# Kernel optimization log

Hardware: AMD Instinct MI355X
Metric: run time of the kernel (lower is better)

The kernel has to match this reference:

```python
import jax, jax.numpy as jnp
import numpy as np

TOPK = 8
NUM_EXPERT_GROUP = 8
TOPK_GROUP = 4
ROUTED_SCALING_FACTOR = 2.5

NUM_TOKENS = 131072
NUM_EXPERTS = 256


def setup_inputs() -> dict:
    key = jax.random.key(0)
    k1, k2 = jax.random.split(key)
    router_logits = jax.random.normal(k1, (NUM_TOKENS, NUM_EXPERTS), dtype=jnp.float32)
    correction_bias = jax.random.normal(k2, (NUM_EXPERTS,), dtype=jnp.float32)
    return {"router_logits": router_logits, "correction_bias": correction_bias}


def reference(router_logits, correction_bias):
    # Biased grouped top-k router (DeepSeek-V3 style), faithful to TopK.__call__
    logits = router_logits.astype(jnp.float32)          # [T, E]
    T, E = logits.shape
    G = NUM_EXPERT_GROUP
    experts_per_group = E // G

    scores_for_choice = logits + correction_bias[None, :]            # [T, E]
    scores_grouped = scores_for_choice.reshape(T, G, experts_per_group)
    # group score = sum of top-2 biased scores in each group
    group_scores = jnp.sum(jax.lax.top_k(scores_grouped, k=2)[0], axis=-1)  # [T, G]
    group_idx = jax.lax.top_k(group_scores, k=TOPK_GROUP)[1]                 # [T, KG]
    group_mask = jnp.clip(jax.nn.one_hot(group_idx, G).sum(axis=1), 0, 1)    # [T, G]
    score_mask = jnp.broadcast_to(group_mask[:, :, None], (T, G, experts_per_group)).reshape(T, E)
    tmp_scores = jnp.where(score_mask.astype(bool), scores_for_choice, float("-inf"))
    topk_ids = jax.lax.top_k(tmp_scores, k=TOPK)[1]                          # [T, K]
    # weights are gathered from the UNbiased logits
    topk_weights = jnp.take_along_axis(logits, topk_ids, axis=1)             # [T, K]
    # renormalize + routed scaling factor
    topk_weights = topk_weights / jnp.sum(topk_weights, axis=-1, keepdims=True)
    topk_weights = topk_weights * ROUTED_SCALING_FACTOR
    return topk_weights.astype(jnp.float32), topk_ids
```

## Files before the change

### kernel.cpp

```cpp
#include <hip/hip_runtime.h>
#include <stdint.h>
#include <math.h>

static constexpr int TOPK   = 8;
static constexpr int NGROUP = 8;
static constexpr int TOPKG  = 4;
static constexpr int NEXP   = 256;
static constexpr float RSF  = 2.5f;

static constexpr int DPP_QX1 = 0xB1;
static constexpr int DPP_QX2 = 0x4E;
static constexpr int DPP_HM  = 0x141;
static constexpr int DPP_MIR = 0x140;
static constexpr int DPP_B15 = 0x142;
static constexpr int DPP_B31 = 0x143;

template <int CTRL>
__device__ __forceinline__ float dppmov(float x) {
    int xi = __float_as_int(x);
    return __int_as_float(__builtin_amdgcn_update_dpp(xi, xi, CTRL, 0xF, 0xF, false));
}

__device__ __forceinline__ uint32_t f2sort(float f) {
    uint32_t u = __float_as_uint(f);
    return u ^ ((uint32_t)((int32_t)u >> 31) | 0x80000000u);
}

__global__ __launch_bounds__(256) void router_kernel(
    const float* __restrict__ logits,
    const float* __restrict__ bias,
    float* __restrict__ out_w,
    float* __restrict__ out_id,
    int T)
{
    const int lane  = threadIdx.x & 63;
    const int token = blockIdx.x * (blockDim.x >> 6) + (threadIdx.x >> 6);
    if (token >= T) return;

    const float* row = logits + (size_t)token * NEXP;
    float4 v = ((const float4*)row)[lane];
    float4 b = ((const float4*)bias)[lane];

    const float s0 = v.x + b.x;
    const float s1 = v.y + b.y;
    const float s2 = v.z + b.z;
    const float s3 = v.w + b.w;

    float hi01 = fmaxf(s0, s1), lo01 = fminf(s0, s1);
    float hi23 = fmaxf(s2, s3), lo23 = fminf(s2, s3);
    float m1 = fmaxf(hi01, hi23);
    float m2 = fmaxf(fminf(hi01, hi23), fmaxf(lo01, lo23));
    {
        float o1 = dppmov<DPP_QX1>(m1), o2 = dppmov<DPP_QX1>(m2);
        float n1 = fmaxf(m1, o1);
        float n2 = fmaxf(fminf(m1, o1), fmaxf(m2, o2));
        m1 = n1; m2 = n2;
    }
    {
        float o1 = dppmov<DPP_QX2>(m1), o2 = dppmov<DPP_QX2>(m2);
        float n1 = fmaxf(m1, o1);
        float n2 = fmaxf(fminf(m1, o1), fmaxf(m2, o2));
        m1 = n1; m2 = n2;
    }
    {
        float o1 = dppmov<DPP_HM>(m1), o2 = dppmov<DPP_HM>(m2);
        float n1 = fmaxf(m1, o1);
        float n2 = fmaxf(fminf(m1, o1), fmaxf(m2, o2));
        m1 = n1; m2 = n2;
    }
    const float gscore = m1 + m2;

    const int g = lane >> 3;
    const uint64_t gkey = ((uint64_t)f2sort(gscore) << 32) | (uint32_t)(7 - g);
    int rank = 0;
    #pragma unroll
    for (int j = 0; j < NGROUP; ++j) {
        uint32_t hi = (uint32_t)__builtin_amdgcn_readlane((int)(uint32_t)(gkey >> 32), j << 3);
        uint32_t lo = (uint32_t)__builtin_amdgcn_readlane((int)(uint32_t)gkey,         j << 3);
        uint64_t gj = ((uint64_t)hi << 32) | lo;
        rank += (gj > gkey) ? 1 : 0;
    }
    const bool sel = (rank < TOPKG);

    const float NEG = -INFINITY;
    float c0 = sel ? s0 : NEG;
    float c1 = sel ? s1 : NEG;
    float c2 = sel ? s2 : NEG;
    float c3 = sel ? s3 : NEG;
    const int ebase = lane << 2;

    int myid = 0;
    #pragma unroll
    for (int r = 0; r < TOPK; ++r) {
        float x = fmaxf(fmaxf(c0, c1), fmaxf(c2, c3));
        x = fmaxf(x, dppmov<DPP_QX1>(x));
        x = fmaxf(x, dppmov<DPP_QX2>(x));
        x = fmaxf(x, dppmov<DPP_HM >(x));
        x = fmaxf(x, dppmov<DPP_MIR>(x));
        x = fmaxf(x, dppmov<DPP_B15>(x));
        x = fmaxf(x, dppmov<DPP_B31>(x));
        const float smax = __int_as_float(
            __builtin_amdgcn_readlane(__float_as_int(x), 63));

        int slot = (c0 == smax) ? 0 : (c1 == smax) ? 1 : (c2 == smax) ? 2 : 3;
        int lidx = ebase | slot;
        uint64_t bal = __ballot((c0 == smax) || (c1 == smax) ||
                                (c2 == smax) || (c3 == smax));
        const int wlane = __ffsll((unsigned long long)bal) - 1;
        const int idx   = __builtin_amdgcn_readlane(lidx, wlane);

        myid = (lane == r) ? idx : myid;

        c0 = (ebase == idx    ) ? NEG : c0;
        c1 = (ebase == idx - 1) ? NEG : c1;
        c2 = (ebase == idx - 2) ? NEG : c2;
        c3 = (ebase == idx - 3) ? NEG : c3;
    }

    float w = 0.f;
    if (lane < TOPK) w = row[myid];
    float t = w;
    t += dppmov<DPP_QX1>(t);
    t += dppmov<DPP_QX2>(t);
    t += dppmov<DPP_HM >(t);

    if (lane < TOPK) {
        out_w [(size_t)token * TOPK + lane] = w / t * RSF;
        out_id[(size_t)token * TOPK + lane] = (float)myid;
    }
}

extern "C" void kernel_launch(void* const* d_in, const int* in_sizes, int n_in,
                              void* d_out, int out_size, void* d_ws, size_t ws_size,
                              hipStream_t stream) {
    const float* logits = (const float*)d_in[0];
    const float* bias   = (const float*)d_in[1];
    const int T = in_sizes[0] / NEXP;
    float* out = (float*)d_out;
    float* out_w  = out;
    float* out_id = out + (size_t)T * TOPK;

    const int waves_per_block = 256 / 64;
    const int blocks = (T + waves_per_block - 1) / waves_per_block;
    router_kernel<<<blocks, 256, 0, stream>>>(logits, bias, out_w, out_id, T);
}
```

Before: 239.8 us.

## Pre-sort per-lane scores and use ballot ranking for group selection

Each lane sorts its four biased scores with a small compare-exchange network, so each top-k round only reduces the lane's head value and shifts a packed index register on the winning lane. Group ranking now uses one shuffle plus a ballot and popcount instead of eight pairs of readlanes. The unbiased weight is rebuilt as the selected biased score minus bias[id], which replaces a scattered reload of the logits row with a bias load. This trades some per-lane sorting work for shorter loop bodies. The recovered weight can differ from the reference in the last bits because of float rounding.

After: 218.5 us. 8.9% less time.

```diff
diff --git a/kernel.cpp b/kernel.cpp
--- a/kernel.cpp
+++ b/kernel.cpp
@@ -3,7 +3,6 @@
 #include <math.h>
 
 static constexpr int TOPK   = 8;
-static constexpr int NGROUP = 8;
 static constexpr int TOPKG  = 4;
 static constexpr int NEXP   = 256;
 static constexpr float RSF  = 2.5f;
@@ -21,9 +20,11 @@
     return __int_as_float(__builtin_amdgcn_update_dpp(xi, xi, CTRL, 0xF, 0xF, false));
 }
 
-__device__ __forceinline__ uint32_t f2sort(float f) {
-    uint32_t u = __float_as_uint(f);
-    return u ^ ((uint32_t)((int32_t)u >> 31) | 0x80000000u);
+__device__ __forceinline__ void cas(float& ax, float& ay, int& ix, int& iy) {
+    bool p   = ax < ay;
+    float hi = fmaxf(ax, ay), lo = fminf(ax, ay);
+    int   nx = p ? iy : ix,   ny = p ? ix : iy;
+    ax = hi; ay = lo; ix = nx; iy = ny;
 }
 
 __global__ __launch_bounds__(256) void router_kernel(
@@ -41,10 +42,10 @@
     float4 v = ((const float4*)row)[lane];
     float4 b = ((const float4*)bias)[lane];
 
-    const float s0 = v.x + b.x;
-    const float s1 = v.y + b.y;
-    const float s2 = v.z + b.z;
-    const float s3 = v.w + b.w;
+    float s0 = v.x + b.x;
+    float s1 = v.y + b.y;
+    float s2 = v.z + b.z;
+    float s3 = v.w + b.w;
 
     float hi01 = fmaxf(s0, s1), lo01 = fminf(s0, s1);
     float hi23 = fmaxf(s2, s3), lo23 = fminf(s2, s3);
@@ -71,28 +72,34 @@
     const float gscore = m1 + m2;
 
     const int g = lane >> 3;
-    const uint64_t gkey = ((uint64_t)f2sort(gscore) << 32) | (uint32_t)(7 - g);
-    int rank = 0;
-    #pragma unroll
-    for (int j = 0; j < NGROUP; ++j) {
-        uint32_t hi = (uint32_t)__builtin_amdgcn_readlane((int)(uint32_t)(gkey >> 32), j << 3);
-        uint32_t lo = (uint32_t)__builtin_amdgcn_readlane((int)(uint32_t)gkey,         j << 3);
-        uint64_t gj = ((uint64_t)hi << 32) | lo;
-        rank += (gj > gkey) ? 1 : 0;
-    }
+    const int j = lane & 7;
+    float gj = __shfl(gscore, j << 3, 64);
+    bool beats = (gj > gscore) || (gj == gscore && j < g);
+    uint64_t bal = __ballot(beats);
+    int rank = __popcll(bal & (0xFFull << (g << 3)));
     const bool sel = (rank < TOPKG);
 
     const float NEG = -INFINITY;
-    float c0 = sel ? s0 : NEG;
-    float c1 = sel ? s1 : NEG;
-    float c2 = sel ? s2 : NEG;
-    float c3 = sel ? s3 : NEG;
+    float a0 = sel ? s0 : NEG;
+    float a1 = sel ? s1 : NEG;
+    float a2 = sel ? s2 : NEG;
+    float a3 = sel ? s3 : NEG;
     const int ebase = lane << 2;
+    int i0 = ebase, i1 = ebase + 1, i2 = ebase + 2, i3 = ebase + 3;
+    cas(a0, a1, i0, i1);
+    cas(a2, a3, i2, i3);
+    cas(a0, a2, i0, i2);
+    cas(a1, a3, i1, i3);
+    cas(a1, a2, i1, i2);
+    uint32_t ipack = (uint32_t)i0 | ((uint32_t)i1 << 8) |
+                     ((uint32_t)i2 << 16) | ((uint32_t)i3 << 24);
+    int i0cur = i0;
 
-    int myid = 0;
+    int   myid = 0;
+    float myw  = 0.f;
     #pragma unroll
     for (int r = 0; r < TOPK; ++r) {
-        float x = fmaxf(fmaxf(c0, c1), fmaxf(c2, c3));
+        float x = a0;
         x = fmaxf(x, dppmov<DPP_QX1>(x));
         x = fmaxf(x, dppmov<DPP_QX2>(x));
         x = fmaxf(x, dppmov<DPP_HM >(x));
@@ -102,23 +109,27 @@
         const float smax = __int_as_float(
             __builtin_amdgcn_readlane(__float_as_int(x), 63));
 
-        int slot = (c0 == smax) ? 0 : (c1 == smax) ? 1 : (c2 == smax) ? 2 : 3;
-        int lidx = ebase | slot;
-        uint64_t bal = __ballot((c0 == smax) || (c1 == smax) ||
-                                (c2 == smax) || (c3 == smax));
-        const int wlane = __ffsll((unsigned long long)bal) - 1;
-        const int idx   = __builtin_amdgcn_readlane(lidx, wlane);
+        uint64_t wb  = __ballot(a0 == smax);
+        const int wl = __ffsll((unsigned long long)wb) - 1;
+        const int idx = __builtin_amdgcn_readlane(i0cur, wl);
 
-        myid = (lane == r) ? idx : myid;
+        const bool mine = (lane == r);
+        myid = mine ? idx  : myid;
+        myw  = mine ? smax : myw;
 
-        c0 = (ebase == idx    ) ? NEG : c0;
-        c1 = (ebase == idx - 1) ? NEG : c1;
-        c2 = (ebase == idx - 2) ? NEG : c2;
-        c3 = (ebase == idx - 3) ? NEG : c3;
+        const bool win = (lane == wl);
+        a0 = win ? a1  : a0;
+        a1 = win ? a2  : a1;
+        a2 = win ? a3  : a2;
+        a3 = win ? NEG : a3;
+        ipack = win ? (ipack >> 8) : ipack;
+        i0cur = (int)(ipack & 255u);
     }
 
-    float w = 0.f;
-    if (lane < TOPK) w = row[myid];
+    float bi = 0.f;
+    if (lane < TOPK) bi = bias[myid];
+    float w = myw - bi;
+
     float t = w;
     t += dppmov<DPP_QX1>(t);
     t += dppmov<DPP_QX2>(t);
```
